# Kernel optimization log

Measured on AMD Instinct MI355X. Metric: run time of the kernel, lower is better.

The kernel has to match this reference:

```python
import jax, jax.numpy as jnp
import numpy as np

EPS = 1e-8
L, D, P, H = 4096, 512, 64, 128


def _div(n, d):
    # torch: d = d*(d>eps) + eps*(d<=eps)
    return n / jnp.where(d > EPS, d, EPS)


def _lstm_last(x, w_ih, w_hh, b_ih, b_hh):
    """Run one LSTM direction over x [L, P], return final hidden state [H]."""
    h_dim = w_hh.shape[1]
    gx = x @ w_ih.T + (b_ih + b_hh)  # [L, 4H], precomputed input contribution

    def step(carry, g):
        h, c = carry
        z = g + h @ w_hh.T
        i, f, gg, o = jnp.split(z, 4)
        c = jax.nn.sigmoid(f) * c + jax.nn.sigmoid(i) * jnp.tanh(gg)
        h = jax.nn.sigmoid(o) * jnp.tanh(c)
        return (h, c), None

    init = (jnp.zeros((h_dim,), x.dtype), jnp.zeros((h_dim,), x.dtype))
    (h_last, _), _ = jax.lax.scan(step, init, gx)
    return h_last


def _multi_perspective(v1, v2, w2):
    """Fused per-perspective weighted cosine similarity.
    v1, v2: [L, D]; w2 = mp_w**2: [P, D]. Returns [L, P].
    cos(w_p*v1, w_p*v2) over D, with torch cosine_similarity eps-clamped norms."""
    num = jnp.einsum('ld,pd,ld->lp', v1, w2, v2)
    n1 = jnp.sqrt(jnp.einsum('ld,pd->lp', v1 * v1, w2))
    n2 = jnp.sqrt(jnp.einsum('ld,pd->lp', v2 * v2, w2))
    return num / (jnp.maximum(n1, EPS) * jnp.maximum(n2, EPS))


def setup_inputs() -> dict:
    key = jax.random.key(0)
    ks = jax.random.split(key, 12)
    lim_w = float(np.sqrt(6.0 / (P + D)))  # xavier_uniform for mp_w
    lim_l = float(1.0 / np.sqrt(H))        # torch LSTM default init
    u = lambda k, shape, lim: jax.random.uniform(k, shape, jnp.float32, -lim, lim)
    return {
        'feature_p': jax.random.normal(ks[0], (L, D), jnp.float32),
        'feature_h': jax.random.normal(ks[1], (L, D), jnp.float32),
        'mp_w': u(ks[2], (P, D), lim_w),
        'w_ih_f': u(ks[3], (4 * H, P), lim_l),
        'w_hh_f': u(ks[4], (4 * H, H), lim_l),
        'b_ih_f': u(ks[5], (4 * H,), lim_l),
        'b_hh_f': u(ks[6], (4 * H,), lim_l),
        'w_ih_r': u(ks[7], (4 * H, P), lim_l),
        'w_hh_r': u(ks[8], (4 * H, H), lim_l),
        'b_ih_r': u(ks[9], (4 * H,), lim_l),
        'b_hh_r': u(ks[10], (4 * H,), lim_l),
    }


def reference(feature_p, feature_h, mp_w, w_ih_f, w_hh_f, b_ih_f, b_hh_f,
              w_ih_r, w_hh_r, b_ih_r, b_hh_r):
    # --- cosine cross-attention (batch of 1, computed unbatched) ---
    a = feature_p @ feature_h.T                                   # [Lp, Lh]
    n_p = jnp.linalg.norm(feature_p, axis=1, keepdims=True)       # [Lp, 1]
    n_h = jnp.linalg.norm(feature_h, axis=1, keepdims=True)       # [Lh, 1]
    att = _div(a, n_p * n_h.T)                                    # [Lp, Lh]

    # --- attention-weighted means (fused: avoids [L,L,D] blow-up) ---
    att_mean_h = _div(att @ feature_h, att.sum(axis=1, keepdims=True))    # [Lp, D]
    att_mean_p = _div(att.T @ feature_p, att.sum(axis=0)[:, None])        # [Lh, D]

    # --- multi-perspective matching (fused weighted cosine) ---
    w2 = mp_w * mp_w
    match_p = _multi_perspective(feature_p, att_mean_h, w2)       # [Lp, P]
    match_h = _multi_perspective(feature_h, att_mean_p, w2)       # [Lh, P]

    # --- BiLSTM aggregation: last hidden state of each direction ---
    def bilstm(x):
        h_f = _lstm_last(x, w_ih_f, w_hh_f, b_ih_f, b_hh_f)
        h_r = _lstm_last(x[::-1], w_ih_r, w_hh_r, b_ih_r, b_hh_r)
        return jnp.concatenate([h_f, h_r])                        # [2H]

    agg_p = bilstm(match_p)
    agg_h = bilstm(match_h)
    return jnp.concatenate([agg_p, agg_h])[None, :]               # [1, 4H]
```

## Files before the change

### kernel.cpp

```cpp
#include <hip/hip_runtime.h>
#include <hip/hip_bf16.h>
#include <math.h>

#define L 4096
#define D 512
#define PP 64
#define HH 128
#define EPSF 1e-8f

typedef _Float16 f16x8 __attribute__((ext_vector_type(8)));
typedef float f32x4 __attribute__((ext_vector_type(4)));
typedef short bf16x8 __attribute__((ext_vector_type(8)));

__device__ __forceinline__ unsigned short f2b(float x) {
  uint32_t u = __float_as_uint(x);
  u += 0x7FFFu + ((u >> 16) & 1u);
  return (unsigned short)(u >> 16);
}
__device__ __forceinline__ float b2f(unsigned short s) {
  return __uint_as_float(((uint32_t)s) << 16);
}

__global__ __launch_bounds__(64) void norms_kernel(const float* __restrict__ fp, const float* __restrict__ fh,
                                                   float* __restrict__ np_, float* __restrict__ nh_) {
  int b = blockIdx.x;
  int which = b >> 12;
  int l = b & (L - 1);
  const float* v = (which ? fh : fp) + (size_t)l * D;
  float s = 0.f;
  for (int i = threadIdx.x; i < D; i += 64) { float x = v[i]; s += x * x; }
  for (int off = 32; off > 0; off >>= 1) s += __shfl_down(s, off);
  if (threadIdx.x == 0) (which ? nh_ : np_)[l] = sqrtf(s);
}

__global__ __launch_bounds__(256) void cast_kernel(const float* __restrict__ fp, const float* __restrict__ fh,
                                                   unsigned short* __restrict__ fpb, unsigned short* __restrict__ fhb) {
  int which = blockIdx.y;
  const float* src = which ? fh : fp;
  unsigned short* dst = which ? fhb : fpb;
  size_t base = ((size_t)blockIdx.x * 256 + threadIdx.x) * 8;
  float4 a = *reinterpret_cast<const float4*>(&src[base]);
  float4 b = *reinterpret_cast<const float4*>(&src[base + 4]);
  unsigned short u[8];
  u[0] = f2b(a.x); u[1] = f2b(a.y); u[2] = f2b(a.z); u[3] = f2b(a.w);
  u[4] = f2b(b.x); u[5] = f2b(b.y); u[6] = f2b(b.z); u[7] = f2b(b.w);
  *reinterpret_cast<uint4*>(&dst[base]) = *reinterpret_cast<uint4*>(u);
}

__global__ __launch_bounds__(256) void transp_kernel(const float* __restrict__ fp, const float* __restrict__ fh,
                                                     unsigned short* __restrict__ fpbt, unsigned short* __restrict__ fhbt) {
  int which = blockIdx.z;
  const float* src = which ? fh : fp;
  unsigned short* dst = which ? fhbt : fpbt;
  __shared__ __align__(16) unsigned short tile[64][68];
  int d0 = blockIdx.x * 64, l0 = blockIdx.y * 64;
  int t = threadIdx.x;
#pragma unroll
  for (int i = 0; i < 4; i++) {
    int idx = t + i * 256;
    int r = idx >> 4, c4 = idx & 15;
    float4 v = *reinterpret_cast<const float4*>(&src[(size_t)(l0 + r) * D + d0 + c4 * 4]);
    unsigned short u[4] = {f2b(v.x), f2b(v.y), f2b(v.z), f2b(v.w)};
    *reinterpret_cast<uint2*>(&tile[r][c4 * 4]) = *reinterpret_cast<uint2*>(u);
  }
  __syncthreads();
#pragma unroll
  for (int i = 0; i < 2; i++) {
    int idx = t + i * 256;
    int dd = idx >> 3, cc = idx & 7;
    unsigned short u[8];
#pragma unroll
    for (int e = 0; e < 8; e++) u[e] = tile[cc * 8 + e][dd];
    *reinterpret_cast<uint4*>(&dst[(size_t)(d0 + dd) * L + l0 + cc * 8]) = *reinterpret_cast<uint4*>(u);
  }
}

__global__ __launch_bounds__(256) void attb_kernel(const unsigned short* __restrict__ fpb,
                                                   const unsigned short* __restrict__ fhb,
                                                   const float* __restrict__ np_, const float* __restrict__ nh_,
                                                   unsigned short* __restrict__ att_b) {
  __shared__ __align__(16) unsigned short As[128][72];
  __shared__ __align__(16) unsigned short Bs[64][72];
  const int t = threadIdx.x, lane = t & 63, wid = t >> 6;
  const int wm = wid >> 1, wn = wid & 1, r = lane & 15, ks = lane >> 4;
  const int row0 = blockIdx.y * 128, col0 = blockIdx.x * 64;
  f32x4 acc[4][2] = {};
  for (int k0 = 0; k0 < D; k0 += 64) {
#pragma unroll
    for (int i = 0; i < 4; i++) {
      int idx = t + i * 256; int row = idx >> 3, c8 = idx & 7;
      uint4 v = *reinterpret_cast<const uint4*>(&fpb[(size_t)(row0 + row) * D + k0 + c8 * 8]);
      *reinterpret_cast<uint4*>(&As[row][c8 * 8]) = v;
    }
#pragma unroll
    for (int i = 0; i < 2; i++) {
      int idx = t + i * 256; int col = idx >> 3, c8 = idx & 7;
      uint4 v = *reinterpret_cast<const uint4*>(&fhb[(size_t)(col0 + col) * D + k0 + c8 * 8]);
      *reinterpret_cast<uint4*>(&Bs[col][c8 * 8]) = v;
    }
    __syncthreads();
#pragma unroll
    for (int k2 = 0; k2 < 2; k2++) {
      bf16x8 b0 = *reinterpret_cast<const bf16x8*>(&Bs[wn * 32 + r][k2 * 32 + ks * 8]);
      bf16x8 b1 = *reinterpret_cast<const bf16x8*>(&Bs[wn * 32 + 16 + r][k2 * 32 + ks * 8]);
#pragma unroll
      for (int fm = 0; fm < 4; fm++) {
        bf16x8 a = *reinterpret_cast<const bf16x8*>(&As[wm * 64 + fm * 16 + r][k2 * 32 + ks * 8]);
        acc[fm][0] = __builtin_amdgcn_mfma_f32_16x16x32_bf16(a, b0, acc[fm][0], 0, 0, 0);
        acc[fm][1] = __builtin_amdgcn_mfma_f32_16x16x32_bf16(a, b1, acc[fm][1], 0, 0, 0);
      }
    }
    __syncthreads();
  }
#pragma unroll
  for (int fm = 0; fm < 4; fm++)
#pragma unroll
    for (int fn = 0; fn < 2; fn++)
#pragma unroll
      for (int reg = 0; reg < 4; reg++) {
        int l = row0 + wm * 64 + fm * 16 + ks * 4 + reg;
        int c = col0 + wn * 32 + fn * 16 + r;
        float den = np_[l] * nh_[c];
        den = den > EPSF ? den : EPSF;
        att_b[(size_t)l * L + c] = f2b(acc[fm][fn][reg] / den);
      }
}

__global__ __launch_bounds__(256) void rowsum_kernel(const unsigned short* __restrict__ att_b, float* __restrict__ rs) {
  int row = blockIdx.x;
  float s = 0.f;
#pragma unroll
  for (int i = 0; i < 2; i++) {
    int chunk = threadIdx.x + i * 256;
    uint4 v = *reinterpret_cast<const uint4*>(&att_b[(size_t)row * L + chunk * 8]);
    const unsigned short* u = reinterpret_cast<const unsigned short*>(&v);
#pragma unroll
    for (int e = 0; e < 8; e++) s += b2f(u[e]);
  }
  for (int off = 32; off > 0; off >>= 1) s += __shfl_down(s, off);
  __shared__ float ps[4];
  if ((threadIdx.x & 63) == 0) ps[threadIdx.x >> 6] = s;
  __syncthreads();
  if (threadIdx.x == 0) rs[row] = ps[0] + ps[1] + ps[2] + ps[3];
}

__global__ __launch_bounds__(256) void colpart_kernel(const unsigned short* __restrict__ att_b, float* __restrict__ pr) {
  int bx = blockIdx.x & 15, by = blockIdx.x >> 4;
  int col = bx * 256 + threadIdx.x;
  int r0 = by * 64;
  float s = 0.f;
#pragma unroll 8
  for (int r = 0; r < 64; r++) s += b2f(att_b[(size_t)(r0 + r) * L + col]);
  pr[(size_t)by * L + col] = s;
}
__global__ __launch_bounds__(256) void colsum_kernel(const float* __restrict__ pr, float* __restrict__ cs) {
  int col = blockIdx.x * 256 + threadIdx.x;
  float s = 0.f;
#pragma unroll 8
  for (int k = 0; k < 64; k++) s += pr[(size_t)k * L + col];
  cs[col] = s;
}

__global__ __launch_bounds__(256) void amh_kernel(const unsigned short* __restrict__ att_b,
                                                  const unsigned short* __restrict__ fhbt,
                                                  const float* __restrict__ rs, float* __restrict__ outm) {
  __shared__ __align__(16) unsigned short As[128][72];
  __shared__ __align__(16) unsigned short Bs[64][72];
  const int t = threadIdx.x, lane = t & 63, wid = t >> 6;
  const int wm = wid >> 1, wn = wid & 1, r = lane & 15, ks = lane >> 4;
  const int row0 = blockIdx.y * 128, col0 = blockIdx.x * 64;
  f32x4 acc[4][2] = {};
  for (int k0 = 0; k0 < L; k0 += 64) {
#pragma unroll
    for (int i = 0; i < 4; i++) {
      int idx = t + i * 256; int row = idx >> 3, c8 = idx & 7;
      uint4 v = *reinterpret_cast<const uint4*>(&att_b[(size_t)(row0 + row) * L + k0 + c8 * 8]);
      *reinterpret_cast<uint4*>(&As[row][c8 * 8]) = v;
    }
#pragma unroll
    for (int i = 0; i < 2; i++) {
      int idx = t + i * 256; int col = idx >> 3, c8 = idx & 7;
      uint4 v = *reinterpret_cast<const uint4*>(&fhbt[(size_t)(col0 + col) * L + k0 + c8 * 8]);
      *reinterpret_cast<uint4*>(&Bs[col][c8 * 8]) = v;
    }
    __syncthreads();
#pragma unroll
    for (int k2 = 0; k2 < 2; k2++) {
      bf16x8 b0 = *reinterpret_cast<const bf16x8*>(&Bs[wn * 32 + r][k2 * 32 + ks * 8]);
      bf16x8 b1 = *reinterpret_cast<const bf16x8*>(&Bs[wn * 32 + 16 + r][k2 * 32 + ks * 8]);
#pragma unroll
      for (int fm = 0; fm < 4; fm++) {
        bf16x8 a = *reinterpret_cast<const bf16x8*>(&As[wm * 64 + fm * 16 + r][k2 * 32 + ks * 8]);
        acc[fm][0] = __builtin_amdgcn_mfma_f32_16x16x32_bf16(a, b0, acc[fm][0], 0, 0, 0);
        acc[fm][1] = __builtin_amdgcn_mfma_f32_16x16x32_bf16(a, b1, acc[fm][1], 0, 0, 0);
      }
    }
    __syncthreads();
  }
#pragma unroll
  for (int fm = 0; fm < 4; fm++)
#pragma unroll
    for (int fn = 0; fn < 2; fn++)
#pragma unroll
      for (int reg = 0; reg < 4; reg++) {
        int l = row0 + wm * 64 + fm * 16 + ks * 4 + reg;
        int d = col0 + wn * 32 + fn * 16 + r;
        float den = rs[l];
        den = den > EPSF ? den : EPSF;
        outm[(size_t)l * D + d] = acc[fm][fn][reg] / den;
      }
}

__global__ __launch_bounds__(256) void amp_kernel(const unsigned short* __restrict__ att_b,
                                                  const unsigned short* __restrict__ fpbt,
                                                  const float* __restrict__ cs, float* __restrict__ outm) {
  __shared__ __align__(16) unsigned short At[128 * 72];
  __shared__ __align__(16) unsigned short Bs[64][72];
  const int t = threadIdx.x, lane = t & 63, wid = t >> 6;
  const int wm = wid >> 1, wn = wid & 1, r = lane & 15, ks = lane >> 4;
  const int row0 = blockIdx.y * 128, col0 = blockIdx.x * 64;
  f32x4 acc[4][2] = {};
  for (int k0 = 0; k0 < L; k0 += 64) {
#pragma unroll
    for (int i = 0; i < 4; i++) {
      int idx = t + i * 256;
      int kk = idx >> 4, c8 = idx & 15;
      uint4 v = *reinterpret_cast<const uint4*>(&att_b[(size_t)(k0 + kk) * L + row0 + c8 * 8]);
      const unsigned short* u = reinterpret_cast<const unsigned short*>(&v);
      int swz = (c8 & 7) << 3;
#pragma unroll
      for (int e = 0; e < 8; e++)
        At[(c8 * 8 + e) * 72 + (kk ^ swz)] = u[e];
    }
#pragma unroll
    for (int i = 0; i < 2; i++) {
      int idx = t + i * 256; int col = idx >> 3, c8 = idx & 7;
      uint4 v = *reinterpret_cast<const uint4*>(&fpbt[(size_t)(col0 + col) * L + k0 + c8 * 8]);
      *reinterpret_cast<uint4*>(&Bs[col][c8 * 8]) = v;
    }
    __syncthreads();
#pragma unroll
    for (int k2 = 0; k2 < 2; k2++) {
      bf16x8 b0 = *reinterpret_cast<const bf16x8*>(&Bs[wn * 32 + r][k2 * 32 + ks * 8]);
      bf16x8 b1 = *reinterpret_cast<const bf16x8*>(&Bs[wn * 32 + 16 + r][k2 * 32 + ks * 8]);
#pragma unroll
      for (int fm = 0; fm < 4; fm++) {
        int j = wm * 64 + fm * 16 + r;
        int off = (k2 * 32 + ks * 8) ^ (((j >> 3) & 7) << 3);
        bf16x8 a = *reinterpret_cast<const bf16x8*>(&At[j * 72 + off]);
        acc[fm][0] = __builtin_amdgcn_mfma_f32_16x16x32_bf16(a, b0, acc[fm][0], 0, 0, 0);
        acc[fm][1] = __builtin_amdgcn_mfma_f32_16x16x32_bf16(a, b1, acc[fm][1], 0, 0, 0);
      }
    }
    __syncthreads();
  }
#pragma unroll
  for (int fm = 0; fm < 4; fm++)
#pragma unroll
    for (int fn = 0; fn < 2; fn++)
#pragma unroll
      for (int reg = 0; reg < 4; reg++) {
        int j = row0 + wm * 64 + fm * 16 + ks * 4 + reg;
        int d = col0 + wn * 32 + fn * 16 + r;
        float den = cs[j];
        den = den > EPSF ? den : EPSF;
        outm[(size_t)j * D + d] = acc[fm][fn][reg] / den;
      }
}

__global__ void w2t_kernel(const float* __restrict__ mpw, float* __restrict__ w2t) {
  int o = blockIdx.x * blockDim.x + threadIdx.x;
  if (o >= PP * D) return;
  int dd = o >> 6, p = o & 63;
  float v = mpw[(size_t)p * D + dd];
  w2t[o] = v * v;
}

__global__ __launch_bounds__(64) void match_kernel(const float* __restrict__ fp, const float* __restrict__ fh,
                                                   const float* __restrict__ amh, const float* __restrict__ amp,
                                                   const float* __restrict__ w2t,
                                                   float* __restrict__ match_p, float* __restrict__ match_h) {
  int b = blockIdx.x;
  int which = b >> 12;
  int l = b & (L - 1);
  const float* v1 = (which ? fh : fp) + (size_t)l * D;
  const float* v2 = (which ? amp : amh) + (size_t)l * D;
  __shared__ float s1[D], s2[D];
  int t = threadIdx.x;
#pragma unroll
  for (int i = 0; i < 2; i++) {
    int f4 = t + 64 * i;
    *reinterpret_cast<float4*>(&s1[f4 * 4]) = *reinterpret_cast<const float4*>(&v1[f4 * 4]);
    *reinterpret_cast<float4*>(&s2[f4 * 4]) = *reinterpret_cast<const float4*>(&v2[f4 * 4]);
  }
  __syncthreads();
  float num = 0.f, a1 = 0.f, a2 = 0.f;
  for (int dd = 0; dd < D; dd++) {
    float wv = w2t[dd * PP + t];
    float x = s1[dd], y = s2[dd];
    num += wv * x * y;
    a1 += wv * x * x;
    a2 += wv * y * y;
  }
  float n1 = fmaxf(sqrtf(a1), EPSF), n2 = fmaxf(sqrtf(a2), EPSF);
  float* outm = which ? match_h : match_p;
  outm[(size_t)l * PP + t] = num / (n1 * n2);
}

__global__ __launch_bounds__(512) void gx_kernel(const float* __restrict__ match_p, const float* __restrict__ match_h,
                                                 const float* __restrict__ wih_f, const float* __restrict__ wih_r,
                                                 const float* __restrict__ bih_f, const float* __restrict__ bhh_f,
                                                 const float* __restrict__ bih_r, const float* __restrict__ bhh_r,
                                                 float* __restrict__ gx) {
  int b = blockIdx.x;
  int dir = b >> 9;
  int chunk = b & 511;
  const float* m_src = (dir < 2) ? match_p : match_h;
  const float* wih = (dir & 1) ? wih_r : wih_f;
  const float* bi = (dir & 1) ? bih_r : bih_f;
  const float* bh = (dir & 1) ? bhh_r : bhh_f;
  __shared__ float m[8][PP];
  int t = threadIdx.x;
  {
    int tt = t >> 6, p = t & 63;
    int tstep = chunk * 8 + tt;
    int row = (dir & 1) ? (L - 1 - tstep) : tstep;
    m[tt][p] = m_src[(size_t)row * PP + p];
  }
  __syncthreads();
  int j = t;
  float bias = bi[j] + bh[j];
  float acc[8];
#pragma unroll
  for (int tt = 0; tt < 8; tt++) acc[tt] = bias;
  for (int p = 0; p < PP; p++) {
    float wv = wih[(size_t)j * PP + p];
#pragma unroll
    for (int tt = 0; tt < 8; tt++) acc[tt] += wv * m[tt][p];
  }
#pragma unroll
  for (int tt = 0; tt < 8; tt++)
    gx[((size_t)dir * L + chunk * 8 + tt) * 512 + j] = acc[tt];
}

__device__ __forceinline__ f16x8 ldw(const float* p) {
  float4 a = *reinterpret_cast<const float4*>(p);
  float4 b = *reinterpret_cast<const float4*>(p + 4);
  f16x8 o;
  o[0] = (_Float16)a.x; o[1] = (_Float16)a.y; o[2] = (_Float16)a.z; o[3] = (_Float16)a.w;
  o[4] = (_Float16)b.x; o[5] = (_Float16)b.y; o[6] = (_Float16)b.z; o[7] = (_Float16)b.w;
  return o;
}

__device__ __forceinline__ void lds_barrier() {
  asm volatile("s_waitcnt lgkmcnt(0)" ::: "memory");
  __builtin_amdgcn_s_barrier();
}

__global__ __attribute__((amdgpu_waves_per_eu(4, 4))) __launch_bounds__(1024)
void lstm_kernel(const float* __restrict__ gx,
                 const float* __restrict__ whh_f, const float* __restrict__ whh_r,
                 float* __restrict__ out) {
  const int dir = blockIdx.x;
  const float* __restrict__ whh = (dir & 1) ? whh_r : whh_f;
  const int tid = threadIdx.x;
  const int lane = tid & 63;
  const int wv = tid >> 6;
  const int r = lane & 15;
  const int ksub = lane >> 4;
  const int jbA = wv * 32;
  const int jbB = wv * 32 + 16;

  const float* baseA = whh + (size_t)(jbA + r) * HH + ksub * 8;
  const float* baseB = whh + (size_t)(jbB + r) * HH + ksub * 8;
  f16x8 wA0 = ldw(baseA);       f16x8 wA1 = ldw(baseA + 32);
  f16x8 wA2 = ldw(baseA + 64);  f16x8 wA3 = ldw(baseA + 96);
  f16x8 wB0 = ldw(baseB);       f16x8 wB1 = ldw(baseB + 32);
  f16x8 wB2 = ldw(baseB + 64);  f16x8 wB3 = ldw(baseB + 96);

  __shared__ __align__(16) _Float16 h_pk[HH];
  __shared__ __align__(16) float z_s[512];
  if (tid < 64) reinterpret_cast<uint32_t*>(h_pk)[tid] = 0u;
  __syncthreads();

  const float* __restrict__ gsrc = gx + (size_t)dir * L * 512;
  const int m = tid & 127;
  const bool phaseB = (tid < HH);
  float c = 0.f, h = 0.f;
  float gi = 0.f, gf = 0.f, gg = 0.f, go = 0.f;
  if (phaseB) {
    gi = gsrc[m]; gf = gsrc[HH + m]; gg = gsrc[2 * HH + m]; go = gsrc[3 * HH + m];
  }
  const char* hp_base = reinterpret_cast<const char*>(h_pk) + ksub * 16;
  const bool col0 = (r == 0);

  for (int t = 0; t < L; t++) {
    float ni = 0.f, nf = 0.f, ng = 0.f, no = 0.f;
    if (phaseB && t + 1 < L) {
      const float* nb = gsrc + (size_t)(t + 1) * 512;
      ni = nb[m]; nf = nb[HH + m]; ng = nb[2 * HH + m]; no = nb[3 * HH + m];
    }
    f32x4 accA = {0.f, 0.f, 0.f, 0.f};
    f32x4 accB = {0.f, 0.f, 0.f, 0.f};
#define CHUNK(q, WA, WB)                                                        \
    {                                                                           \
      uint4 raw = *reinterpret_cast<const uint4*>(hp_base + (q) * 64);          \
      raw.x = col0 ? raw.x : 0u; raw.y = col0 ? raw.y : 0u;                     \
      raw.z = col0 ? raw.z : 0u; raw.w = col0 ? raw.w : 0u;                     \
      f16x8 bf = __builtin_bit_cast(f16x8, raw);                                \
      accA = __builtin_amdgcn_mfma_f32_16x16x32_f16(WA, bf, accA, 0, 0, 0);     \
      accB = __builtin_amdgcn_mfma_f32_16x16x32_f16(WB, bf, accB, 0, 0, 0);     \
    }
    CHUNK(0, wA0, wB0)
    CHUNK(1, wA1, wB1)
    CHUNK(2, wA2, wB2)
    CHUNK(3, wA3, wB3)
#undef CHUNK
    if (col0) {
      float4 zA; zA.x = accA[0]; zA.y = accA[1]; zA.z = accA[2]; zA.w = accA[3];
      float4 zB; zB.x = accB[0]; zB.y = accB[1]; zB.z = accB[2]; zB.w = accB[3];
      *reinterpret_cast<float4*>(&z_s[jbA + ksub * 4]) = zA;
      *reinterpret_cast<float4*>(&z_s[jbB + ksub * 4]) = zB;
    }
    lds_barrier();
    if (phaseB) {
      float zi = z_s[m] + gi;
      float zf = z_s[HH + m] + gf;
      float zg = z_s[2 * HH + m] + gg;
      float zo = z_s[3 * HH + m] + go;
      float iv = 1.f / (1.f + __expf(-zi));
      float fv = 1.f / (1.f + __expf(-zf));
      float eg = __expf(2.f * zg);
      float gvv = 1.f - 2.f / (eg + 1.f);
      float ov = 1.f / (1.f + __expf(-zo));
      c = fv * c + iv * gvv;
      float e2 = __expf(2.f * c);
      h = ov * (1.f - 2.f / (e2 + 1.f));
      h_pk[m] = (_Float16)h;
    }
    lds_barrier();
    gi = ni; gf = nf; gg = ng; go = no;
  }
  if (phaseB) out[dir * HH + tid] = h;
}

extern "C" void kernel_launch(void* const* d_in, const int* in_sizes, int n_in,
                              void* d_out, int out_size, void* d_ws, size_t ws_size,
                              hipStream_t stream) {
  const float* fp    = (const float*)d_in[0];
  const float* fh    = (const float*)d_in[1];
  const float* mpw   = (const float*)d_in[2];
  const float* wih_f = (const float*)d_in[3];
  const float* whh_f = (const float*)d_in[4];
  const float* bih_f = (const float*)d_in[5];
  const float* bhh_f = (const float*)d_in[6];
  const float* wih_r = (const float*)d_in[7];
  const float* whh_r = (const float*)d_in[8];
  const float* bih_r = (const float*)d_in[9];
  const float* bhh_r = (const float*)d_in[10];
  float* out = (float*)d_out;
  float* ws = (float*)d_ws;

  size_t np_off   = 0;
  size_t nh_off   = np_off + L;
  size_t rs_off   = nh_off + L;
  size_t cs_off   = rs_off + L;
  size_t w2_off   = cs_off + L;
  size_t amh_off  = w2_off + (size_t)PP * D;
  size_t amp_off  = amh_off + (size_t)L * D;
  size_t mp_off   = amp_off + (size_t)L * D;
  size_t mh_off   = mp_off + (size_t)L * PP;
  size_t pr_off   = mh_off + (size_t)L * PP;
  size_t fpb_off  = pr_off + (size_t)64 * L;
  size_t fhb_off  = fpb_off + (size_t)L * D / 2;
  size_t fpbt_off = fhb_off + (size_t)L * D / 2;
  size_t fhbt_off = fpbt_off + (size_t)L * D / 2;
  size_t attb_off = fhbt_off + (size_t)L * D / 2;
  size_t gx_off   = attb_off;
  size_t total    = attb_off + (size_t)L * L / 2;
  {
    size_t gx_end = gx_off + (size_t)4 * L * 512;
    if (gx_end > total) total = gx_end;
  }
  if (ws_size < total * sizeof(float)) return;

  float* np_  = ws + np_off;
  float* nh_  = ws + nh_off;
  float* rs   = ws + rs_off;
  float* cs   = ws + cs_off;
  float* w2t  = ws + w2_off;
  float* amh  = ws + amh_off;
  float* amp  = ws + amp_off;
  float* mtp  = ws + mp_off;
  float* mth  = ws + mh_off;
  float* pr   = ws + pr_off;
  unsigned short* fpb  = (unsigned short*)(ws + fpb_off);
  unsigned short* fhb  = (unsigned short*)(ws + fhb_off);
  unsigned short* fpbt = (unsigned short*)(ws + fpbt_off);
  unsigned short* fhbt = (unsigned short*)(ws + fhbt_off);
  unsigned short* attb = (unsigned short*)(ws + attb_off);
  float* gx   = ws + gx_off;

  norms_kernel<<<2 * L, 64, 0, stream>>>(fp, fh, np_, nh_);
  cast_kernel<<<dim3((L * D) / (256 * 8), 2), 256, 0, stream>>>(fp, fh, fpb, fhb);
  transp_kernel<<<dim3(D / 64, L / 64, 2), 256, 0, stream>>>(fp, fh, fpbt, fhbt);
  attb_kernel<<<dim3(L / 64, L / 128), 256, 0, stream>>>(fpb, fhb, np_, nh_, attb);
  rowsum_kernel<<<L, 256, 0, stream>>>(attb, rs);
  colpart_kernel<<<1024, 256, 0, stream>>>(attb, pr);
  colsum_kernel<<<16, 256, 0, stream>>>(pr, cs);
  amh_kernel<<<dim3(D / 64, L / 128), 256, 0, stream>>>(attb, fhbt, rs, amh);
  amp_kernel<<<dim3(D / 64, L / 128), 256, 0, stream>>>(attb, fpbt, cs, amp);
  w2t_kernel<<<(PP * D + 255) / 256, 256, 0, stream>>>(mpw, w2t);
  match_kernel<<<2 * L, 64, 0, stream>>>(fp, fh, amh, amp, w2t, mtp, mth);
  gx_kernel<<<4 * (L / 8), 512, 0, stream>>>(mtp, mth, wih_f, wih_r, bih_f, bhh_f, bih_r, bhh_r, gx);
  lstm_kernel<<<4, 1024, 0, stream>>>(gx, whh_f, whh_r, out);
}
```

Measured before the change: 3.742 ms.

## Replace MFMA recurrent matvec with fp32 register-resident weights and DPP reductions

The LSTM recurrence kernel drops the fp16 MFMA matvec, where most of the output columns were masked to zero. Each lane now holds 8 rows by 8 k-values of W_hh in fp32 registers and computes the partial dot products with FMAs. The partials are combined with DPP lane moves plus one shuffle, so every lane ends up owning one gate pre-activation and applies its sigmoid or tanh before the cell update. This spreads the activation work across all threads, keeps fp32 precision, and shortens the serial per-step critical path, at the cost of more VALU work and register pressure.

Result: faster. 3.523 ms (-5.9%).

```diff
diff --git a/kernel.cpp b/kernel.cpp
--- a/kernel.cpp
+++ b/kernel.cpp
@@ -8,7 +8,6 @@
 #define HH 128
 #define EPSF 1e-8f
 
-typedef _Float16 f16x8 __attribute__((ext_vector_type(8)));
 typedef float f32x4 __attribute__((ext_vector_type(4)));
 typedef short bf16x8 __attribute__((ext_vector_type(8)));
 
@@ -343,18 +342,16 @@
     gx[((size_t)dir * L + chunk * 8 + tt) * 512 + j] = acc[tt];
 }
 
-__device__ __forceinline__ f16x8 ldw(const float* p) {
-  float4 a = *reinterpret_cast<const float4*>(p);
-  float4 b = *reinterpret_cast<const float4*>(p + 4);
-  f16x8 o;
-  o[0] = (_Float16)a.x; o[1] = (_Float16)a.y; o[2] = (_Float16)a.z; o[3] = (_Float16)a.w;
-  o[4] = (_Float16)b.x; o[5] = (_Float16)b.y; o[6] = (_Float16)b.z; o[7] = (_Float16)b.w;
-  return o;
-}
-
-__device__ __forceinline__ void lds_barrier() {
-  asm volatile("s_waitcnt lgkmcnt(0)" ::: "memory");
-  __builtin_amdgcn_s_barrier();
+__device__ __forceinline__ float4 load4_opaque(const float* p) {
+  float4 v;
+  asm volatile("global_load_dwordx4 %0, %1, off\n\ts_waitcnt vmcnt(0)"
+               : "=v"(v) : "v"(p));
+  return v;
+}
+
+template <int CTRL>
+__device__ __forceinline__ float xdpp(float x) {
+  return __int_as_float(__builtin_amdgcn_mov_dpp(__float_as_int(x), CTRL, 0xf, 0xf, true));
 }
 
 __global__ __attribute__((amdgpu_waves_per_eu(4, 4))) __launch_bounds__(1024)
@@ -366,82 +363,89 @@
   const int tid = threadIdx.x;
   const int lane = tid & 63;
   const int wv = tid >> 6;
-  const int r = lane & 15;
-  const int ksub = lane >> 4;
-  const int jbA = wv * 32;
-  const int jbB = wv * 32 + 16;
-
-  const float* baseA = whh + (size_t)(jbA + r) * HH + ksub * 8;
-  const float* baseB = whh + (size_t)(jbB + r) * HH + ksub * 8;
-  f16x8 wA0 = ldw(baseA);       f16x8 wA1 = ldw(baseA + 32);
-  f16x8 wA2 = ldw(baseA + 64);  f16x8 wA3 = ldw(baseA + 96);
-  f16x8 wB0 = ldw(baseB);       f16x8 wB1 = ldw(baseB + 32);
-  f16x8 wB2 = ldw(baseB + 64);  f16x8 wB3 = ldw(baseB + 96);
-
-  __shared__ __align__(16) _Float16 h_pk[HH];
-  __shared__ __align__(16) float z_s[512];
-  if (tid < 64) reinterpret_cast<uint32_t*>(h_pk)[tid] = 0u;
+  const int sec = lane >> 4;
+  const int gam = lane & 15;
+  const int o_of = (gam & 1) | (((gam >> 1) & 1) << 1) | (((gam >> 3) & 1) << 2);
+  const int jsec = wv * 32 + sec * 8;
+  const int jmine = jsec + o_of;
+  const int kbase = gam * 8;
+
+  float4 w4[8][2];
+#pragma unroll
+  for (int jj = 0; jj < 8; jj++) {
+    w4[jj][0] = load4_opaque(&whh[(size_t)(jsec + jj) * HH + kbase]);
+    w4[jj][1] = load4_opaque(&whh[(size_t)(jsec + jj) * HH + kbase + 4]);
+  }
+
+  __shared__ __align__(16) float h_pad[16 * 12];
+  __shared__ float act[512];
+  if (tid < 192) h_pad[tid] = 0.f;
   __syncthreads();
 
   const float* __restrict__ gsrc = gx + (size_t)dir * L * 512;
+  float gval = gsrc[jmine];
   const int m = tid & 127;
-  const bool phaseB = (tid < HH);
+  const int is_g_gate = ((jmine >> 7) == 2);
+  const int s0b = gam & 1, s1b = gam & 2, s3b = gam & 8;
+  const int hoff = gam * 12;
+  const int hwr = (m >> 3) * 12 + (m & 7);
   float c = 0.f, h = 0.f;
-  float gi = 0.f, gf = 0.f, gg = 0.f, go = 0.f;
-  if (phaseB) {
-    gi = gsrc[m]; gf = gsrc[HH + m]; gg = gsrc[2 * HH + m]; go = gsrc[3 * HH + m];
-  }
-  const char* hp_base = reinterpret_cast<const char*>(h_pk) + ksub * 16;
-  const bool col0 = (r == 0);
 
   for (int t = 0; t < L; t++) {
-    float ni = 0.f, nf = 0.f, ng = 0.f, no = 0.f;
-    if (phaseB && t + 1 < L) {
-      const float* nb = gsrc + (size_t)(t + 1) * 512;
-      ni = nb[m]; nf = nb[HH + m]; ng = nb[2 * HH + m]; no = nb[3 * HH + m];
-    }
-    f32x4 accA = {0.f, 0.f, 0.f, 0.f};
-    f32x4 accB = {0.f, 0.f, 0.f, 0.f};
-#define CHUNK(q, WA, WB)                                                        \
-    {                                                                           \
-      uint4 raw = *reinterpret_cast<const uint4*>(hp_base + (q) * 64);          \
-      raw.x = col0 ? raw.x : 0u; raw.y = col0 ? raw.y : 0u;                     \
-      raw.z = col0 ? raw.z : 0u; raw.w = col0 ? raw.w : 0u;                     \
-      f16x8 bf = __builtin_bit_cast(f16x8, raw);                                \
-      accA = __builtin_amdgcn_mfma_f32_16x16x32_f16(WA, bf, accA, 0, 0, 0);     \
-      accB = __builtin_amdgcn_mfma_f32_16x16x32_f16(WB, bf, accB, 0, 0, 0);     \
-    }
-    CHUNK(0, wA0, wB0)
-    CHUNK(1, wA1, wB1)
-    CHUNK(2, wA2, wB2)
-    CHUNK(3, wA3, wB3)
-#undef CHUNK
-    if (col0) {
-      float4 zA; zA.x = accA[0]; zA.y = accA[1]; zA.z = accA[2]; zA.w = accA[3];
-      float4 zB; zB.x = accB[0]; zB.y = accB[1]; zB.z = accB[2]; zB.w = accB[3];
-      *reinterpret_cast<float4*>(&z_s[jbA + ksub * 4]) = zA;
-      *reinterpret_cast<float4*>(&z_s[jbB + ksub * 4]) = zB;
-    }
-    lds_barrier();
-    if (phaseB) {
-      float zi = z_s[m] + gi;
-      float zf = z_s[HH + m] + gf;
-      float zg = z_s[2 * HH + m] + gg;
-      float zo = z_s[3 * HH + m] + go;
-      float iv = 1.f / (1.f + __expf(-zi));
-      float fv = 1.f / (1.f + __expf(-zf));
-      float eg = __expf(2.f * zg);
-      float gvv = 1.f - 2.f / (eg + 1.f);
-      float ov = 1.f / (1.f + __expf(-zo));
-      c = fv * c + iv * gvv;
+    float gnext = (t + 1 < L) ? gsrc[(size_t)(t + 1) * 512 + jmine] : 0.f;
+    float4 hf0 = *reinterpret_cast<const float4*>(&h_pad[hoff]);
+    float4 hf1 = *reinterpret_cast<const float4*>(&h_pad[hoff + 4]);
+    float acc[8];
+#pragma unroll
+    for (int jj = 0; jj < 8; jj++) {
+      float s0 = w4[jj][0].x * hf0.x;
+      float s1 = w4[jj][0].y * hf0.y;
+      s0 = fmaf(w4[jj][0].z, hf0.z, s0);
+      s1 = fmaf(w4[jj][0].w, hf0.w, s1);
+      s0 = fmaf(w4[jj][1].x, hf1.x, s0);
+      s1 = fmaf(w4[jj][1].y, hf1.y, s1);
+      s0 = fmaf(w4[jj][1].z, hf1.z, s0);
+      s1 = fmaf(w4[jj][1].w, hf1.w, s1);
+      acc[jj] = s0 + s1;
+    }
+    float r4[4];
+#pragma unroll
+    for (int i = 0; i < 4; i++) {
+      float keep = s0b ? acc[2 * i + 1] : acc[2 * i];
+      float send = s0b ? acc[2 * i] : acc[2 * i + 1];
+      r4[i] = keep + xdpp<0xB1>(send);
+    }
+    float r2[2];
+#pragma unroll
+    for (int u = 0; u < 2; u++) {
+      float keep = s1b ? r4[2 * u + 1] : r4[2 * u];
+      float send = s1b ? r4[2 * u] : r4[2 * u + 1];
+      r2[u] = keep + xdpp<0x4E>(send);
+    }
+    float keep1 = s3b ? r2[1] : r2[0];
+    float send1 = s3b ? r2[0] : r2[1];
+    float r1 = keep1 + xdpp<0x128>(send1);
+    float z = r1 + __shfl_xor(r1, 4) + gval;
+    float a;
+    if (is_g_gate) {
+      float e = __expf(2.f * z);
+      a = 1.f - 2.f / (e + 1.f);
+    } else {
+      a = 1.f / (1.f + __expf(-z));
+    }
+    act[jmine] = a;
+    __syncthreads();
+    if (tid < HH) {
+      float iv = act[m], fv = act[HH + m], gg = act[2 * HH + m], ov = act[3 * HH + m];
+      c = fv * c + iv * gg;
       float e2 = __expf(2.f * c);
       h = ov * (1.f - 2.f / (e2 + 1.f));
-      h_pk[m] = (_Float16)h;
-    }
-    lds_barrier();
-    gi = ni; gf = nf; gg = ng; go = no;
-  }
-  if (phaseB) out[dir * HH + tid] = h;
+      h_pad[hwr] = h;
+    }
+    __syncthreads();
+    gval = gnext;
+  }
+  if (tid < HH) out[dir * HH + tid] = h;
 }
 
 extern "C" void kernel_launch(void* const* d_in, const int* in_sizes, int n_in,
```
